# Optimization experiments

Hardware: AMD Instinct MI355X
Metric: run time of the kernel (lower is better)

The kernel has to match this reference:

```python
import jax, jax.numpy as jnp
import numpy as np
import math

B, NS, NT = 8, 512, 512
NSRC, NTRG = B * NS, B * NT
E = 32768
SCALAR_DIM, EMBED, ORI, LAYERS, K, KK = 20, 128, 1024, 3, 5, 25
CONV_IN = 2 * EMBED
FINAL_IN = ORI + LAYERS * EMBED


def sinusoidal_pos_emb(x):
    half = SCALAR_DIM // 2
    freqs = jnp.exp(-(math.log(10000.0) / (half - 1)) * jnp.arange(half, dtype=x.dtype))
    ang = x[:, None] * freqs[None, :]
    return jnp.concatenate([jnp.sin(ang), jnp.cos(ang)], axis=-1)


def spline_basis(pseudo):
    # open B-spline basis, degree 1, kernel_size K per dim, dim=2 (torch_spline_conv semantics)
    v = pseudo * (K - 1)
    lo = jnp.floor(v)
    frac = v - lo
    lo = lo.astype(jnp.int32)
    idxs, ws = [], []
    for s1 in (0, 1):
        for s0 in (0, 1):
            i0 = jnp.clip(lo[:, 0] + s0, 0, K - 1)
            i1 = jnp.clip(lo[:, 1] + s1, 0, K - 1)
            w0 = frac[:, 0] if s0 else 1.0 - frac[:, 0]
            w1 = frac[:, 1] if s1 else 1.0 - frac[:, 1]
            idxs.append(i0 + K * i1)
            ws.append(w0 * w1)
    idx = jnp.stack(idxs, 1)  # [E,4] kernel indices
    w = jnp.stack(ws, 1)      # [E,4] basis weights
    e = pseudo.shape[0]
    # dense [E,KK] coefficient matrix (<=4 nonzeros per row)
    return jnp.zeros((e, KK), pseudo.dtype).at[jnp.arange(e)[:, None], idx].add(w)


def spline_conv(x, edge_index, edge_attr, W, root, bias):
    # SplineConv(in=CONV_IN, out=EMBED, dim=2, kernel_size=5, degree=1, aggr='mean', root_weight=True)
    src, dst = edge_index[0], edge_index[1]
    x_j = x[src]                    # [E, in] gather of source features
    C = spline_basis(edge_attr)     # [E, KK]
    msg = jnp.zeros((x_j.shape[0], W.shape[-1]), x.dtype)
    for k in range(KK):             # fixed small kernel loop (25 GEMMs)
        msg = msg + (C[:, k:k + 1] * x_j) @ W[k]
    n = x.shape[0]
    agg = jax.ops.segment_sum(msg, dst, num_segments=n)
    deg = jax.ops.segment_sum(jnp.ones((msg.shape[0],), x.dtype), dst, num_segments=n)
    agg = agg / jnp.clip(deg, 1.0)[:, None]   # mean aggregation
    return agg + x @ root + bias


def masked_softmax(src, mask):
    out = jnp.where(mask, src, -jnp.inf)
    out = jax.nn.softmax(out, axis=-1)
    return jnp.where(mask, out, 0.0)


def setup_inputs() -> dict:
    key = jax.random.key(0)
    ks = jax.random.split(key, 16)
    s = 0.02
    # block-diagonal edges: both endpoints within the same graph
    gs = jax.random.randint(ks[11], (E,), 0, B)
    gt = jax.random.randint(ks[12], (E,), 0, B)
    ei_s = jnp.stack([gs * NS + jax.random.randint(ks[13], (E,), 0, NS),
                      gs * NS + jax.random.randint(ks[14], (E,), 0, NS)])
    ei_t = jnp.stack([gt * NT + jax.random.randint(ks[15], (E,), 0, NT),
                      gt * NT + jax.random.randint(ks[0], (E,), 0, NT)])
    return {
        "t": jax.random.uniform(ks[1], (B,)),
        "Xt": jax.random.uniform(ks[2], (B, NS, NT)),
        "x_s": jax.random.normal(ks[3], (NSRC, ORI)),
        "x_t": jax.random.normal(ks[4], (NTRG, ORI)),
        "ea_s": jax.random.uniform(ks[5], (E, 2)),
        "ea_t": jax.random.uniform(ks[6], (E, 2)),
        "lin0_w": jax.random.normal(ks[7], (ORI + 2 * SCALAR_DIM, EMBED)) * s,
        "lin0_b": jnp.zeros((EMBED,)),
        "lin_w": jax.random.normal(ks[8], (LAYERS - 1, EMBED + 2 * SCALAR_DIM, EMBED)) * s,
        "lin_b": jnp.zeros((LAYERS - 1, EMBED)),
        "conv_w": jax.random.normal(ks[9], (LAYERS, KK, CONV_IN, EMBED)) * s,
        "conv_root": jax.random.normal(ks[10], (LAYERS, CONV_IN, EMBED)) * s,
        "conv_bias": jnp.zeros((LAYERS, EMBED)),
        "final_w": jax.random.normal(jax.random.fold_in(key, 99), (FINAL_IN, EMBED)) * s,
        "final_b": jnp.zeros((EMBED,)),
        "ei_s": ei_s,
        "ei_t": ei_t,
        "s_mask": jnp.ones((B, NS), dtype=bool),
        "t_mask": jnp.ones((B, NT), dtype=bool),
        "mask_align": jnp.ones((B, NS, NT), dtype=bool),
    }


def reference(t, Xt, x_s, x_t, ea_s, ea_t, lin0_w, lin0_b, lin_w, lin_b,
              conv_w, conv_root, conv_bias, final_w, final_b,
              ei_s, ei_t, s_mask, t_mask, mask_align):
    # All graphs have exactly NS/NT nodes, so s_mask/t_mask are all-True:
    # boolean select x[s_mask] == reshape, and to_dense_batch == reshape.
    time_emb = sinusoidal_pos_emb(t)                                    # [B, 20]
    num_src = sinusoidal_pos_emb(Xt.sum(-1).reshape(-1) / 10.0)         # [NSRC, 20]
    num_trg = sinusoidal_pos_emb(jnp.swapaxes(Xt, 1, 2).sum(-1).reshape(-1) / 10.0)
    tf_src = jnp.repeat(time_emb, NS, axis=0)                           # per-node time features
    tf_trg = jnp.repeat(time_emb, NT, axis=0)
    xs_src, xs_trg = [x_s], [x_t]
    for i in range(LAYERS):
        w = lin0_w if i == 0 else lin_w[i - 1]
        b = lin0_b if i == 0 else lin_b[i - 1]
        xin_s = jnp.concatenate([xs_src[-1], num_src, tf_src], -1) @ w + b
        xin_t = jnp.concatenate([xs_trg[-1], num_trg, tf_trg], -1) @ w + b
        xp_s = xin_s.reshape(B, NS, EMBED)
        xp_t = xin_t.reshape(B, NT, EMBED)
        tgt_msg = jnp.einsum('bst,btd->bsd', Xt, xp_t)
        src_msg = jnp.einsum('bst,bsd->btd', Xt, xp_s)
        diff_s = (xp_s - tgt_msg).reshape(NSRC, EMBED)
        diff_t = (xp_t - src_msg).reshape(NTRG, EMBED)
        cat_s = jnp.concatenate([xin_s, diff_s], -1)
        cat_t = jnp.concatenate([xin_t, diff_t], -1)
        xs_src.append(jnp.tanh(spline_conv(cat_s, ei_s, ea_s, conv_w[i], conv_root[i], conv_bias[i])))
        xs_trg.append(jnp.tanh(spline_conv(cat_t, ei_t, ea_t, conv_w[i], conv_root[i], conv_bias[i])))
    h_s = jnp.concatenate(xs_src, -1) @ final_w + final_b
    h_t = jnp.concatenate(xs_trg, -1) @ final_w + final_b
    sim = jnp.einsum('bsd,btd->bst', h_s.reshape(B, NS, EMBED), h_t.reshape(B, NT, EMBED))
    return masked_softmax(sim, mask_align).reshape(NSRC, NT)
```

## Files before the change

### kernel.cpp

```cpp
#include <hip/hip_runtime.h>
#include <hip/hip_bf16.h>

typedef __hip_bfloat16 hb;
typedef short short8 __attribute__((ext_vector_type(8)));
typedef float f32x4 __attribute__((ext_vector_type(4)));
typedef unsigned short u16;

#define NNODE 4096
#define NEDGE 32768
#define EMB   128
#define ORI   1024
#define SD    20
#define CIN   256
#define NCV   3328

__device__ __forceinline__ float b2f(hb v){ return __bfloat162float(v); }
__device__ __forceinline__ hb f2b(float v){ return __float2bfloat16(v); }

__device__ __forceinline__ void split2(float x, u16& hi, u16& lo){
  hb h = f2b(x);
  float r = x - b2f(h);
  hb l = f2b(r);
  __builtin_memcpy(&hi, &h, 2);
  __builtin_memcpy(&lo, &l, 2);
}

__device__ __forceinline__ void gl16(const void* g, void* l){
  __builtin_amdgcn_global_load_lds(
      (const __attribute__((address_space(1))) unsigned int*)(size_t)g,
      (__attribute__((address_space(3))) unsigned int*)(unsigned int)(size_t)l,
      16, 0, 0);
}


__global__ __launch_bounds__(256) void k_rowsum(const float* __restrict__ Xt, float* __restrict__ rowsum){
  int row = blockIdx.x*4 + (threadIdx.x >> 6);
  int lane = threadIdx.x & 63;
  const float* p = Xt + (size_t)row*512;
  float s = 0.f;
  for (int i = lane; i < 512; i += 64) s += p[i];
  for (int off = 32; off; off >>= 1) s += __shfl_xor(s, off);
  if (lane == 0) rowsum[row] = s;
}

__global__ __launch_bounds__(256) void k_colsum(const float* __restrict__ Xt, float* __restrict__ colsum){
  int col = blockIdx.x*256 + threadIdx.x;
  int b = col >> 9, t = col & 511;
  const float* p = Xt + (size_t)b*512*512 + t;
  float s = 0.f;
  for (int sidx = 0; sidx < 512; ++sidx) s += p[(size_t)sidx*512];
  colsum[col] = s;
}

__global__ void k_posemb(const float* __restrict__ vals, int n, float scale, float* __restrict__ out){
  int i = blockIdx.x*blockDim.x + threadIdx.x;
  if (i >= n) return;
  float x = vals[i]*scale;
  float c = -logf(10000.f)/9.f;
  for (int j = 0; j < 10; ++j) {
    float f = expf(c*(float)j);
    out[i*20 + j]      = sinf(x*f);
    out[i*20 + 10 + j] = cosf(x*f);
  }
}

__global__ void k_basis2(const float* __restrict__ ea_s, const float* __restrict__ ea_t,
                         int* __restrict__ idx4, float* __restrict__ w4){
  int e = blockIdx.x*256 + threadIdx.x;
  const float* ea = (e < NEDGE) ? ea_s : ea_t;
  int el = e & (NEDGE-1);
  float p0 = ea[el*2]   * 4.0f;
  float p1 = ea[el*2+1] * 4.0f;
  float l0 = floorf(p0), l1 = floorf(p1);
  float f0 = p0 - l0, f1 = p1 - l1;
  int i0 = (int)l0, i1 = (int)l1;
  int j = 0;
  for (int s1 = 0; s1 <= 1; ++s1)
    for (int s0 = 0; s0 <= 1; ++s0) {
      int a  = min(max(i0 + s0, 0), 4);
      int bb = min(max(i1 + s1, 0), 4);
      float w = (s0 ? f0 : 1.f - f0) * (s1 ? f1 : 1.f - f1);
      idx4[e*4 + j] = a + 5*bb;
      w4[e*4 + j] = w;
      ++j;
    }
}

__global__ void k_count2(const int* __restrict__ ds, const int* __restrict__ dt, int* __restrict__ cnt){
  int e = blockIdx.x*256 + threadIdx.x;
  int side = e >= NEDGE;
  int el = e & (NEDGE-1);
  int node = (side ? dt : ds)[el];
  atomicAdd(&cnt[side*NNODE + node], 1);
}

__global__ __launch_bounds__(256) void k_scan2(const int* __restrict__ cntAll, int* __restrict__ rowptrAll,
                                               int* __restrict__ eposAll, float* __restrict__ invAll){
  int sideOff = blockIdx.x*NNODE;
  const int* cnt = cntAll + sideOff;
  int* rowptr = rowptrAll + blockIdx.x*(NNODE+1);
  int* epos = eposAll + sideOff;
  float* inv = invAll + sideOff;
  __shared__ int part[256];
  int tid = threadIdx.x;
  int base = tid*16;
  int v[16]; int s = 0;
  #pragma unroll
  for (int i = 0; i < 16; ++i){
    v[i] = s; int c = cnt[base+i]; s += c;
    inv[base+i] = 1.f / fmaxf((float)c, 1.f);
  }
  part[tid] = s; __syncthreads();
  int total = s;
  for (int off = 1; off < 256; off <<= 1){
    int y = (tid >= off) ? part[tid-off] : 0;
    __syncthreads();
    part[tid] += y;
    __syncthreads();
  }
  int excl = part[tid] - total;
  #pragma unroll
  for (int i = 0; i < 16; ++i){ int r = excl + v[i]; rowptr[base+i] = r; epos[base+i] = r; }
  if (tid == 255) rowptr[4096] = part[255];
}

__global__ void k_fill2(const int* __restrict__ ds, const int* __restrict__ dt,
                        int* __restrict__ eposAll, int* __restrict__ elistAll){
  int e = blockIdx.x*256 + threadIdx.x;
  int side = e >= NEDGE;
  int el = e & (NEDGE-1);
  int node = (side ? dt : ds)[el];
  int p = atomicAdd(&eposAll[side*NNODE + node], 1);
  elistAll[side*NEDGE + p] = el;
}

__global__ __launch_bounds__(256) void k_xtT2(const float* __restrict__ Xt,
    u16* __restrict__ XH, u16* __restrict__ XL, u16* __restrict__ TH, u16* __restrict__ TL){
  __shared__ float tile[64][65];
  int b = blockIdx.z, s0 = blockIdx.y*64, t0 = blockIdx.x*64;
  const float* src = Xt + (size_t)b*262144;
  size_t ob = (size_t)b*262144;
  #pragma unroll 4
  for (int p = 0; p < 16; ++p) {
    int idx = p*256 + threadIdx.x;
    int r = idx >> 6, c = idx & 63;
    float v = src[(size_t)(s0+r)*512 + t0 + c];
    tile[r][c] = v;
    size_t o = ob + (size_t)(s0+r)*512 + t0 + c;
    split2(v, XH[o], XL[o]);
  }
  __syncthreads();
  #pragma unroll 4
  for (int p = 0; p < 16; ++p) {
    int idx = p*256 + threadIdx.x;
    int r = idx >> 6, c = idx & 63;
    float v = tile[c][r];
    size_t o = ob + (size_t)(t0+r)*512 + s0 + c;
    split2(v, TH[o], TL[o]);
  }
}

__global__ void k_wT2(const float* __restrict__ src, u16* __restrict__ dH, u16* __restrict__ dL,
                      int Krows, int ldDst){
  int i = blockIdx.x*256 + threadIdx.x;
  if (i >= 128*ldDst) return;
  int n = i / ldDst, k = i - n*ldDst;
  float v = (k < Krows) ? src[(size_t)k*128 + n] : 0.f;
  split2(v, dH[i], dL[i]);
}

__global__ void k_wc2(const float* __restrict__ convw, const float* __restrict__ root,
                      u16* __restrict__ dH, u16* __restrict__ dL){
  int i = blockIdx.x*256 + threadIdx.x;
  int l = i / (NCV*CIN);
  int r = i - l*(NCV*CIN);
  int k = r & 255, n = r >> 8;
  const float* cw = convw + (size_t)l*25*CIN*128;
  const float* rt = root  + (size_t)l*CIN*128;
  float v;
  if (n < 3200) { int kk = n >> 7, col = n & 127; v = cw[((size_t)kk*256 + k)*128 + col]; }
  else          { int col = n & 127;              v = rt[(size_t)k*128 + col]; }
  split2(v, dH[i], dL[i]);
}

__global__ void k_aux2(const float* __restrict__ nums, const float* __restrict__ numt,
                       const float* __restrict__ temb, u16* __restrict__ aH, u16* __restrict__ aL){
  int i = blockIdx.x*256 + threadIdx.x;
  if (i >= 8192*64) return;
  int r = i >> 6, c = i & 63;
  int side = r >> 12, local = r & 4095, b = (r >> 9) & 7;
  float v = 0.f;
  if (c < 20) v = (side ? numt : nums)[local*20 + c];
  else if (c < 40) v = temb[b*20 + (c - 20)];
  split2(v, aH[i], aL[i]);
}

__global__ __launch_bounds__(256) void k_split(const float* __restrict__ src,
    u16* __restrict__ dH, u16* __restrict__ dL, int n){
  int i = blockIdx.x*256 + threadIdx.x;
  if (i < n) split2(src[i], dH[i], dL[i]);
}

__global__ __launch_bounds__(256) void k_xinT(const float* __restrict__ src,
    u16* __restrict__ dH, u16* __restrict__ dL, float* __restrict__ cat){
  __shared__ float tile[64][65];
  int r0 = blockIdx.x*64, c0 = blockIdx.y*64;
  #pragma unroll 4
  for (int p = 0; p < 16; ++p) {
    int idx = p*256 + threadIdx.x;
    int r = idx >> 6, c = idx & 63;
    float v = src[(size_t)(r0+r)*128 + c0 + c];
    tile[r][c] = v;
    cat[(size_t)(r0+r)*256 + c0 + c]       = v;
    cat[(size_t)(r0+r)*256 + 128 + c0 + c] = v;
  }
  __syncthreads();
  #pragma unroll 4
  for (int p = 0; p < 16; ++p) {
    int idx = p*256 + threadIdx.x;
    int r = idx >> 6, c = idx & 63;
    float v = tile[c][r];
    size_t o = (size_t)(c0+r)*8192 + r0 + c;
    split2(v, dH[o], dL[o]);
  }
}

__global__ __launch_bounds__(256) void k_fillbias(const float* __restrict__ b, float* __restrict__ o){
  int i = blockIdx.x*256 + threadIdx.x;
  o[i] = b[i & 127];
}

__global__ __launch_bounds__(256) void k_gemm(
    const u16* __restrict__ Ah, const u16* __restrict__ Al, int lda, long aBatch,
    const u16* __restrict__ Bh, const u16* __restrict__ Bl, int ldb, long bBatch,
    int K, int flags, int ksplit,
    float* __restrict__ outF, const float* __restrict__ bias,
    int ldo, int oRowOff, int oBatchRows, const float* __restrict__ X)
{
  __shared__ __align__(16) u16 S[2][4][4096];
  const int tid = threadIdx.x;
  const int ln = tid & 63, w = tid >> 6;
  const int wm = (w >> 1)*64, wn = (w & 1)*64;
  const int l15 = ln & 15, q = ln >> 4;
  const int by = blockIdx.y, bz = blockIdx.z;
  const int batch = bz / ksplit;
  const int kidx  = bz - batch*ksplit;
  const int bxm = blockIdx.x;
  const int kSteps = K >> 5;
  const int spc = (kSteps + ksplit - 1) / ksplit;
  const int kBeg = kidx * spc * 32;
  const int kEnd = min(K, kBeg + spc*32);
  if (kBeg >= kEnd) return;
  const u16* Abh = Ah + (size_t)batch*aBatch + (size_t)bxm*128*lda;
  const u16* Abl = Al + (size_t)batch*aBatch + (size_t)bxm*128*lda;
  const u16* Bbh = Bh + (size_t)batch*bBatch + (size_t)by*128*ldb;
  const u16* Bbl = Bl + (size_t)batch*bBatch + (size_t)by*128*ldb;

  f32x4 acc[4][4];
  #pragma unroll
  for (int i = 0; i < 4; ++i)
    #pragma unroll
    for (int j = 0; j < 4; ++j) acc[i][j] = (f32x4){0.f,0.f,0.f,0.f};

  const int r0 = w*32 + (ln >> 2);
  const int r1 = r0 + 16;
  const int c0 = ((ln & 3) ^ ((r0 >> 1) & 3)) * 8;
  const int c1 = ((ln & 3) ^ ((r1 >> 1) & 3)) * 8;

  auto stage = [&](int buf, int kc){
    char* wb = (char*)&S[buf][0][0] + w*2048;
    size_t gA0 = (size_t)r0*lda + kc + c0;
    size_t gA1 = (size_t)r1*lda + kc + c1;
    size_t gB0 = (size_t)r0*ldb + kc + c0;
    size_t gB1 = (size_t)r1*ldb + kc + c1;
    gl16(Abh + gA0, wb);           gl16(Abh + gA1, wb + 1024);
    gl16(Abl + gA0, wb + 8192);    gl16(Abl + gA1, wb + 9216);
    gl16(Bbh + gB0, wb + 16384);   gl16(Bbh + gB1, wb + 17408);
    gl16(Bbl + gB0, wb + 24576);   gl16(Bbl + gB1, wb + 25600);
  };

  auto compute = [&](int buf){
    const u16* AhS = &S[buf][0][0]; const u16* AlS = &S[buf][1][0];
    const u16* BhS = &S[buf][2][0]; const u16* BlS = &S[buf][3][0];
    short8 ah[4], al[4], bh[4], bl[4];
    #pragma unroll
    for (int i = 0; i < 4; ++i) {
      int ra = wm + i*16 + l15;
      int oa = ra*32 + ((q ^ ((ra >> 1) & 3)) << 3);
      ah[i] = *(const short8*)&AhS[oa];
      al[i] = *(const short8*)&AlS[oa];
      int rb = wn + i*16 + l15;
      int ob = rb*32 + ((q ^ ((rb >> 1) & 3)) << 3);
      bh[i] = *(const short8*)&BhS[ob];
      bl[i] = *(const short8*)&BlS[ob];
    }
    #pragma unroll
    for (int i = 0; i < 4; ++i)
      #pragma unroll
      for (int j = 0; j < 4; ++j) {
        acc[i][j] = __builtin_amdgcn_mfma_f32_16x16x32_bf16(ah[i], bl[j], acc[i][j], 0, 0, 0);
        acc[i][j] = __builtin_amdgcn_mfma_f32_16x16x32_bf16(al[i], bh[j], acc[i][j], 0, 0, 0);
        acc[i][j] = __builtin_amdgcn_mfma_f32_16x16x32_bf16(ah[i], bh[j], acc[i][j], 0, 0, 0);
      }
  };

  stage(0, kBeg);
  __syncthreads();
  int cur = 0;
  for (int kc = kBeg; kc < kEnd; kc += 32) {
    if (kc + 32 < kEnd) stage(cur ^ 1, kc + 32);
    compute(cur);
    __syncthreads();
    cur ^= 1;
  }

  const int rowBase = oRowOff + batch*oBatchRows + bxm*128;
  #pragma unroll
  for (int i = 0; i < 4; ++i) {
    #pragma unroll
    for (int j = 0; j < 4; ++j) {
      int col = by*128 + wn + j*16 + l15;
      #pragma unroll
      for (int r = 0; r < 4; ++r) {
        int row = rowBase + wm + i*16 + q*4 + r;
        float v = acc[i][j][r];
        if (flags & 8) {
          if (flags & 4) unsafeAtomicAdd(&outF[(size_t)row*256 + 128 + col], -v);
          else           unsafeAtomicAdd(&outF[(size_t)row*ldo + col], v);
        } else {
          if (flags & 2) v += bias[col];
          if (flags & 1) v += outF[(size_t)row*ldo + col];
          if (flags & 4) {
            float xv = X[(size_t)row*128 + col];
            outF[(size_t)row*256 + col]       = xv;
            outF[(size_t)row*256 + 128 + col] = xv - v;
          } else {
            outF[(size_t)row*ldo + col] = v;
          }
        }
      }
    }
  }
}

__global__ __launch_bounds__(128) void k_aggtanh(const float* __restrict__ Y,
    const int* __restrict__ srcarr, const int* __restrict__ elist, const int* __restrict__ rowptr,
    const int* __restrict__ idx4, const float* __restrict__ w4, const float* __restrict__ inv,
    const float* __restrict__ bias, u16* __restrict__ xsH, u16* __restrict__ xsL){
  int node = blockIdx.x, tid = threadIdx.x;
  float acc = Y[(size_t)node*NCV + 3200 + tid];
  float wi = inv[node];
  int beg = rowptr[node], end = rowptr[node+1];
  for (int p = beg; p < end; ++p) {
    int e = elist[p];
    int sn = srcarr[e];
    const float* yrow = Y + (size_t)sn*NCV;
    #pragma unroll
    for (int j = 0; j < 4; ++j) {
      int k = idx4[e*4+j];
      float w = w4[e*4+j]*wi;
      acc += w * yrow[k*128 + tid];
    }
  }
  float r = tanhf(acc + bias[tid]);
  split2(r, xsH[(size_t)node*EMB + tid], xsL[(size_t)node*EMB + tid]);
}

__global__ __launch_bounds__(256) void k_softmax(const float* __restrict__ sim, float* __restrict__ out){
  int row = blockIdx.x, tid = threadIdx.x;
  __shared__ float red[8];
  float v0 = sim[(size_t)row*512 + tid];
  float v1 = sim[(size_t)row*512 + 256 + tid];
  int wid = tid >> 6, lane = tid & 63;
  float m = fmaxf(v0, v1);
  for (int off = 32; off; off >>= 1) m = fmaxf(m, __shfl_xor(m, off));
  if (lane == 0) red[wid] = m;
  __syncthreads();
  if (tid == 0) red[4] = fmaxf(fmaxf(red[0], red[1]), fmaxf(red[2], red[3]));
  __syncthreads();
  m = red[4];
  float e0 = expf(v0 - m), e1 = expf(v1 - m);
  float s = e0 + e1;
  for (int off = 32; off; off >>= 1) s += __shfl_xor(s, off);
  if (lane == 0) red[wid] = s;
  __syncthreads();
  if (tid == 0) red[5] = red[0] + red[1] + red[2] + red[3];
  __syncthreads();
  float inv = 1.f / red[5];
  out[(size_t)row*512 + tid]       = e0*inv;
  out[(size_t)row*512 + 256 + tid] = e1*inv;
}


extern "C" void kernel_launch(void* const* d_in, const int* in_sizes, int n_in,
                              void* d_out, int out_size, void* d_ws, size_t ws_size,
                              hipStream_t stream){
  (void)in_sizes; (void)n_in; (void)out_size; (void)ws_size;
  const float* t_in      = (const float*)d_in[0];
  const float* Xt        = (const float*)d_in[1];
  const float* x_s       = (const float*)d_in[2];
  const float* x_t       = (const float*)d_in[3];
  const float* ea_s      = (const float*)d_in[4];
  const float* ea_t      = (const float*)d_in[5];
  const float* lin0_w    = (const float*)d_in[6];
  const float* lin0_b    = (const float*)d_in[7];
  const float* lin_w     = (const float*)d_in[8];
  const float* lin_b     = (const float*)d_in[9];
  const float* conv_w    = (const float*)d_in[10];
  const float* conv_root = (const float*)d_in[11];
  const float* conv_bias = (const float*)d_in[12];
  const float* final_w   = (const float*)d_in[13];
  const float* final_b   = (const float*)d_in[14];
  const int*   ei_s      = (const int*)d_in[15];
  const int*   ei_t      = (const int*)d_in[16];
  float* out = (float*)d_out;

  char* wsb = (char*)d_ws;
  size_t off = 0;
  auto alloc = [&](size_t bytes)->char*{
    char* p = wsb + off;
    off += (bytes + 255) & ~(size_t)255;
    return p;
  };
  float* f_sums  = (float*)alloc(8192*4);
  float* f_temb  = (float*)alloc(8*SD*4);
  float* f_num   = (float*)alloc((size_t)8192*SD*4);
  int*   i_idx   = (int*)  alloc((size_t)2*NEDGE*4*4);
  float* f_w     = (float*)alloc((size_t)2*NEDGE*4*4);
  int*   i_cnt   = (int*)  alloc((size_t)2*NNODE*4);
  float* f_inv   = (float*)alloc((size_t)2*NNODE*4);
  int*   i_rp    = (int*)  alloc((size_t)2*(NNODE+1)*4);
  int*   i_ep    = (int*)  alloc((size_t)2*NNODE*4);
  int*   i_el    = (int*)  alloc((size_t)2*NEDGE*4);
  u16* XtH  = (u16*)alloc((size_t)8*512*512*2);
  u16* XtL  = (u16*)alloc((size_t)8*512*512*2);
  u16* XtTH = (u16*)alloc((size_t)8*512*512*2);
  u16* XtTL = (u16*)alloc((size_t)8*512*512*2);
  u16* w0H  = (u16*)alloc((size_t)128*1088*2);
  u16* w0L  = (u16*)alloc((size_t)128*1088*2);
  u16* w1H  = (u16*)alloc((size_t)128*192*2);
  u16* w1L  = (u16*)alloc((size_t)128*192*2);
  u16* w2H  = (u16*)alloc((size_t)128*192*2);
  u16* w2L  = (u16*)alloc((size_t)128*192*2);
  u16* wfH  = (u16*)alloc((size_t)128*1408*2);
  u16* wfL  = (u16*)alloc((size_t)128*1408*2);
  u16* wcH  = (u16*)alloc((size_t)3*NCV*CIN*2);
  u16* wcL  = (u16*)alloc((size_t)3*NCV*CIN*2);
  u16* auxH = (u16*)alloc((size_t)8192*64*2);
  u16* auxL = (u16*)alloc((size_t)8192*64*2);
  u16* xH   = (u16*)alloc((size_t)8192*1024*2);
  u16* xL   = (u16*)alloc((size_t)8192*1024*2);
  u16* xsH[3]; u16* xsL[3];
  for (int l = 0; l < 3; ++l) {
    xsH[l] = (u16*)alloc((size_t)8192*EMB*2);
    xsL[l] = (u16*)alloc((size_t)8192*EMB*2);
  }
  u16* catH = (u16*)alloc((size_t)8192*CIN*2);
  u16* catL = (u16*)alloc((size_t)8192*CIN*2);
  float* f_xin = (float*)alloc((size_t)8192*EMB*4);
  float* f_cat = (float*)alloc((size_t)8192*CIN*4);
  float* f_Y   = (float*)alloc((size_t)NNODE*NCV*4);
  float* f_sim = f_Y;
  u16* xiTH = (u16*)((char*)f_Y + (size_t)20*1024*1024);
  u16* xiTL = (u16*)((char*)f_Y + (size_t)23*1024*1024);
  u16* hH   = (u16*)((char*)f_Y + (size_t)26*1024*1024);
  u16* hL   = (u16*)((char*)f_Y + (size_t)29*1024*1024);

  auto gemm = [&](const u16* Ahp, const u16* Alp, int lda, long aB,
                  const u16* Bhp, const u16* Blp, int ldb, long bB,
                  int K, int flags, int ksplit, float* o, const float* bias,
                  int ldo, int rowOff, int oBR, const float* X, dim3 grid){
    k_gemm<<<grid, 256, 0, stream>>>(Ahp, Alp, lda, aB, Bhp, Blp, ldb, bB, K, flags, ksplit,
                                     o, bias, ldo, rowOff, oBR, X);
  };

  k_xtT2<<<dim3(8,8,8), 256, 0, stream>>>(Xt, XtH, XtL, XtTH, XtTL);
  k_rowsum<<<NNODE/4, 256, 0, stream>>>(Xt, f_sums);
  k_colsum<<<NNODE/256, 256, 0, stream>>>(Xt, f_sums + NNODE);
  k_posemb<<<8192/256, 256, 0, stream>>>(f_sums, 8192, 0.1f, f_num);
  k_posemb<<<1, 64, 0, stream>>>(t_in, 8, 1.0f, f_temb);
  k_aux2<<<(8192*64)/256, 256, 0, stream>>>(f_num, f_num + (size_t)NNODE*SD, f_temb, auxH, auxL);
  k_basis2<<<2*NEDGE/256, 256, 0, stream>>>(ea_s, ea_t, i_idx, f_w);
  hipMemsetAsync(i_cnt, 0, 2*NNODE*4, stream);
  k_count2<<<2*NEDGE/256, 256, 0, stream>>>(ei_s + NEDGE, ei_t + NEDGE, i_cnt);
  k_scan2<<<2, 256, 0, stream>>>(i_cnt, i_rp, i_ep, f_inv);
  k_fill2<<<2*NEDGE/256, 256, 0, stream>>>(ei_s + NEDGE, ei_t + NEDGE, i_ep, i_el);
  k_wT2<<<(128*1088)/256, 256, 0, stream>>>(lin0_w, w0H, w0L, 1064, 1088);
  k_wT2<<<(128*192)/256, 256, 0, stream>>>(lin_w, w1H, w1L, 168, 192);
  k_wT2<<<(128*192)/256, 256, 0, stream>>>(lin_w + (size_t)168*128, w2H, w2L, 168, 192);
  k_wT2<<<(128*1408)/256, 256, 0, stream>>>(final_w, wfH, wfL, 1408, 1408);
  k_wc2<<<(3*NCV*CIN)/256, 256, 0, stream>>>(conv_w, conv_root, wcH, wcL);
  k_split<<<(4096*1024)/256, 256, 0, stream>>>(x_s, xH, xL, 4096*1024);
  k_split<<<(4096*1024)/256, 256, 0, stream>>>(x_t, xH + (size_t)4096*1024, xL + (size_t)4096*1024, 4096*1024);

  for (int i = 0; i < 3; ++i) {
    const u16* wTh = (i == 0) ? w0H : (i == 1) ? w1H : w2H;
    const u16* wTl = (i == 0) ? w0L : (i == 1) ? w1L : w2L;
    const float* bv = (i == 0) ? lin0_b : lin_b + (i-1)*EMB;
    int ldw = (i == 0) ? 1088 : 192;
    int Kx  = (i == 0) ? 1024 : 128;

    gemm(auxH, auxL, 64, 0, wTh + Kx, wTl + Kx, ldw, 0,
         64, 2, 1, f_xin, bv, EMB, 0, 0, nullptr, dim3(64,1,1));
    const u16* A0h = (i == 0) ? xH : xsH[i-1];
    const u16* A0l = (i == 0) ? xL : xsL[i-1];
    int ks = (i == 0) ? 8 : 4;
    gemm(A0h, A0l, Kx, 0, wTh, wTl, ldw, 0,
         Kx, 8, ks, f_xin, nullptr, EMB, 0, 0, nullptr, dim3(64,1,ks));

    k_xinT<<<dim3(128,2), 256, 0, stream>>>(f_xin, xiTH, xiTL, f_cat);
    gemm(XtH, XtL, 512, 262144, xiTH + 4096, xiTL + 4096, 8192, 512,
         512, 4|8, 8, f_cat, nullptr, 256, 0, 512, f_xin, dim3(4,1,64));
    gemm(XtTH, XtTL, 512, 262144, xiTH, xiTL, 8192, 512,
         512, 4|8, 8, f_cat, nullptr, 256, NNODE, 512, f_xin, dim3(4,1,64));
    k_split<<<(8192*CIN)/256, 256, 0, stream>>>(f_cat, catH, catL, 8192*CIN);

    for (int side = 0; side < 2; ++side) {
      gemm(catH + (size_t)side*NNODE*CIN, catL + (size_t)side*NNODE*CIN, CIN, 0,
           wcH + (size_t)i*NCV*CIN, wcL + (size_t)i*NCV*CIN, CIN, 0,
           CIN, 0, 1, f_Y, nullptr, NCV, 0, 0, nullptr, dim3(32,26,1));
      k_aggtanh<<<NNODE, 128, 0, stream>>>(f_Y,
          side ? ei_t : ei_s, i_el + side*NEDGE, i_rp + side*(NNODE+1),
          i_idx + (size_t)side*NEDGE*4, f_w + (size_t)side*NEDGE*4, f_inv + side*NNODE,
          conv_bias + i*EMB,
          xsH[i] + (size_t)side*NNODE*EMB, xsL[i] + (size_t)side*NNODE*EMB);
    }
  }

  float* f_h = f_xin;
  k_fillbias<<<4096, 256, 0, stream>>>(final_b, f_h);
  gemm(xH, xL, 1024, 0, wfH, wfL, 1408, 0,
       1024, 8, 8, f_h, nullptr, EMB, 0, 0, nullptr, dim3(64,1,8));
  for (int l = 0; l < 3; ++l)
    gemm(xsH[l], xsL[l], 128, 0, wfH + 1024 + l*128, wfL + 1024 + l*128, 1408, 0,
         128, 8, 4, f_h, nullptr, EMB, 0, 0, nullptr, dim3(64,1,4));
  k_split<<<(8192*EMB)/256, 256, 0, stream>>>(f_h, hH, hL, 8192*EMB);

  gemm(hH, hL, EMB, 65536, hH + (size_t)4096*EMB, hL + (size_t)4096*EMB, EMB, 65536,
       EMB, 0, 1, f_sim, nullptr, 512, 0, 512, nullptr, dim3(4,4,8));

  k_softmax<<<NNODE, 256, 0, stream>>>(f_sim, out);
}
```

Before: 930.3 us.

## Merge paired Xt GEMMs into one launch, split-K sim GEMM, pack aggtanh blocks

The GEMM kernel gains an optional second A/B operand set, so the source and target message GEMMs run in a single launch with a doubled z-grid. The final similarity GEMM now uses split-K 4 with atomic accumulation into a zeroed buffer, giving it more blocks. The aggregation kernel handles two nodes per 256-thread block. These cut launch count and raise occupancy, at the cost of an extra memset and more atomic traffic.

Result: slower. 949.4 us (+2.1%).

```diff
diff --git a/kernel.cpp b/kernel.cpp
--- a/kernel.cpp
+++ b/kernel.cpp
@@ -235,14 +235,24 @@
     const u16* __restrict__ Bh, const u16* __restrict__ Bl, int ldb, long bBatch,
     int K, int flags, int ksplit,
     float* __restrict__ outF, const float* __restrict__ bias,
-    int ldo, int oRowOff, int oBatchRows, const float* __restrict__ X)
+    int ldo, int oRowOff, int oBatchRows, const float* __restrict__ X,
+    const u16* __restrict__ A2h, const u16* __restrict__ A2l,
+    const u16* __restrict__ B2h, const u16* __restrict__ B2l, int oRowOff2)
 {
   __shared__ __align__(16) u16 S[2][4][4096];
   const int tid = threadIdx.x;
   const int ln = tid & 63, w = tid >> 6;
   const int wm = (w >> 1)*64, wn = (w & 1)*64;
   const int l15 = ln & 15, q = ln >> 4;
-  const int by = blockIdx.y, bz = blockIdx.z;
+  const int by = blockIdx.y;
+  int bz = blockIdx.z;
+  const u16* Aph = Ah; const u16* Apl = Al;
+  const u16* Bph = Bh; const u16* Bpl = Bl;
+  int rowOffSel = oRowOff;
+  if (B2h != nullptr) {
+    int half = gridDim.z >> 1;
+    if (bz >= half) { bz -= half; Aph = A2h; Apl = A2l; Bph = B2h; Bpl = B2l; rowOffSel = oRowOff2; }
+  }
   const int batch = bz / ksplit;
   const int kidx  = bz - batch*ksplit;
   const int bxm = blockIdx.x;
@@ -251,10 +261,10 @@
   const int kBeg = kidx * spc * 32;
   const int kEnd = min(K, kBeg + spc*32);
   if (kBeg >= kEnd) return;
-  const u16* Abh = Ah + (size_t)batch*aBatch + (size_t)bxm*128*lda;
-  const u16* Abl = Al + (size_t)batch*aBatch + (size_t)bxm*128*lda;
-  const u16* Bbh = Bh + (size_t)batch*bBatch + (size_t)by*128*ldb;
-  const u16* Bbl = Bl + (size_t)batch*bBatch + (size_t)by*128*ldb;
+  const u16* Abh = Aph + (size_t)batch*aBatch + (size_t)bxm*128*lda;
+  const u16* Abl = Apl + (size_t)batch*aBatch + (size_t)bxm*128*lda;
+  const u16* Bbh = Bph + (size_t)batch*bBatch + (size_t)by*128*ldb;
+  const u16* Bbl = Bpl + (size_t)batch*bBatch + (size_t)by*128*ldb;
 
   f32x4 acc[4][4];
   #pragma unroll
@@ -314,7 +324,7 @@
     cur ^= 1;
   }
 
-  const int rowBase = oRowOff + batch*oBatchRows + bxm*128;
+  const int rowBase = rowOffSel + batch*oBatchRows + bxm*128;
   #pragma unroll
   for (int i = 0; i < 4; ++i) {
     #pragma unroll
@@ -343,11 +353,12 @@
   }
 }
 
-__global__ __launch_bounds__(128) void k_aggtanh(const float* __restrict__ Y,
+__global__ __launch_bounds__(256) void k_aggtanh(const float* __restrict__ Y,
     const int* __restrict__ srcarr, const int* __restrict__ elist, const int* __restrict__ rowptr,
     const int* __restrict__ idx4, const float* __restrict__ w4, const float* __restrict__ inv,
     const float* __restrict__ bias, u16* __restrict__ xsH, u16* __restrict__ xsL){
-  int node = blockIdx.x, tid = threadIdx.x;
+  int node = blockIdx.x*2 + (threadIdx.x >> 7);
+  int tid = threadIdx.x & 127;
   float acc = Y[(size_t)node*NCV + 3200 + tid];
   float wi = inv[node];
   int beg = rowptr[node], end = rowptr[node+1];
@@ -469,9 +480,12 @@
   auto gemm = [&](const u16* Ahp, const u16* Alp, int lda, long aB,
                   const u16* Bhp, const u16* Blp, int ldb, long bB,
                   int K, int flags, int ksplit, float* o, const float* bias,
-                  int ldo, int rowOff, int oBR, const float* X, dim3 grid){
+                  int ldo, int rowOff, int oBR, const float* X, dim3 grid,
+                  const u16* A2h = nullptr, const u16* A2l = nullptr,
+                  const u16* B2h = nullptr, const u16* B2l = nullptr, int rowOff2 = 0){
     k_gemm<<<grid, 256, 0, stream>>>(Ahp, Alp, lda, aB, Bhp, Blp, ldb, bB, K, flags, ksplit,
-                                     o, bias, ldo, rowOff, oBR, X);
+                                     o, bias, ldo, rowOff, oBR, X,
+                                     A2h, A2l, B2h, B2l, rowOff2);
   };
 
   k_xtT2<<<dim3(8,8,8), 256, 0, stream>>>(Xt, XtH, XtL, XtTH, XtTL);
@@ -510,16 +524,15 @@
 
     k_xinT<<<dim3(128,2), 256, 0, stream>>>(f_xin, xiTH, xiTL, f_cat);
     gemm(XtH, XtL, 512, 262144, xiTH + 4096, xiTL + 4096, 8192, 512,
-         512, 4|8, 8, f_cat, nullptr, 256, 0, 512, f_xin, dim3(4,1,64));
-    gemm(XtTH, XtTL, 512, 262144, xiTH, xiTL, 8192, 512,
-         512, 4|8, 8, f_cat, nullptr, 256, NNODE, 512, f_xin, dim3(4,1,64));
+         512, 4|8, 8, f_cat, nullptr, 256, 0, 512, nullptr, dim3(4,1,128),
+         XtTH, XtTL, xiTH, xiTL, NNODE);
     k_split<<<(8192*CIN)/256, 256, 0, stream>>>(f_cat, catH, catL, 8192*CIN);
 
     for (int side = 0; side < 2; ++side) {
       gemm(catH + (size_t)side*NNODE*CIN, catL + (size_t)side*NNODE*CIN, CIN, 0,
            wcH + (size_t)i*NCV*CIN, wcL + (size_t)i*NCV*CIN, CIN, 0,
            CIN, 0, 1, f_Y, nullptr, NCV, 0, 0, nullptr, dim3(32,26,1));
-      k_aggtanh<<<NNODE, 128, 0, stream>>>(f_Y,
+      k_aggtanh<<<NNODE/2, 256, 0, stream>>>(f_Y,
           side ? ei_t : ei_s, i_el + side*NEDGE, i_rp + side*(NNODE+1),
           i_idx + (size_t)side*NEDGE*4, f_w + (size_t)side*NEDGE*4, f_inv + side*NNODE,
           conv_bias + i*EMB,
@@ -536,8 +549,9 @@
          128, 8, 4, f_h, nullptr, EMB, 0, 0, nullptr, dim3(64,1,4));
   k_split<<<(8192*EMB)/256, 256, 0, stream>>>(f_h, hH, hL, 8192*EMB);
 
+  hipMemsetAsync(f_sim, 0, (size_t)4096*512*4, stream);
   gemm(hH, hL, EMB, 65536, hH + (size_t)4096*EMB, hL + (size_t)4096*EMB, EMB, 65536,
-       EMB, 0, 1, f_sim, nullptr, 512, 0, 512, nullptr, dim3(4,4,8));
+       EMB, 8, 4, f_sim, nullptr, 512, 0, 512, nullptr, dim3(4,4,32));
 
   k_softmax<<<NNODE, 256, 0, stream>>>(f_sim, out);
 }
```
